# Kernel optimization log

Measured on AMD Instinct MI355X. Metric: run time of the kernel, lower is better.

Reference implementation:

```python
import jax, jax.numpy as jnp
import numpy as np

EMBED_DIM = 768
NUM_HEADS = 12


def setup_inputs() -> dict:
    key = jax.random.key(0)
    ks = jax.random.split(key, 9)
    C = EMBED_DIM
    x = jax.random.normal(ks[0], (8, 3136, C), dtype=jnp.float32)
    s = 0.02
    Wq = jax.random.normal(ks[1], (C, C), dtype=jnp.float32) * s
    Wk = jax.random.normal(ks[2], (C, C), dtype=jnp.float32) * s
    Wv = jax.random.normal(ks[3], (C, C), dtype=jnp.float32) * s
    Wo = jax.random.normal(ks[4], (C, C), dtype=jnp.float32) * s
    bq = jax.random.normal(ks[5], (C,), dtype=jnp.float32) * s
    bk = jax.random.normal(ks[6], (C,), dtype=jnp.float32) * s
    bv = jax.random.normal(ks[7], (C,), dtype=jnp.float32) * s
    bo = jax.random.normal(ks[8], (C,), dtype=jnp.float32) * s
    return {"x": x, "Wq": Wq, "bq": bq, "Wk": Wk, "bk": bk,
            "Wv": Wv, "bv": bv, "Wo": Wo, "bo": bo, "T": 16}


def reference(x, Wq, bq, Wk, bk, Wv, bv, Wo, bo, T):
    B, N, C = x.shape
    H = NUM_HEADS
    hd = C // H
    Hh = H // 2
    P = N // T
    scale = 1.0 / np.sqrt(hd).astype(np.float32)

    Q = (x @ Wq + bq).reshape(B, T, P, H, hd)
    K = (x @ Wk + bk).reshape(B, T, P, H, hd)
    V = (x @ Wv + bv).reshape(B, T, P, H, hd)

    # spatial attention: first Hh heads, attend over patches within each frame
    Qs, Ks, Vs = Q[..., :Hh, :], K[..., :Hh, :], V[..., :Hh, :]
    scores_s = jnp.einsum('btphd,btqhd->bthpq', Qs, Ks) * scale  # (B,T,Hh,P,P)
    ws = jax.nn.softmax(scores_s, axis=-1)
    out_s = jnp.einsum('bthpq,btqhd->btphd', ws, Vs)  # (B,T,P,Hh,hd)

    # temporal attention: last Hh heads, attend over frames at each patch
    Qt, Kt, Vt = Q[..., Hh:, :], K[..., Hh:, :], V[..., Hh:, :]
    scores_t = jnp.einsum('btphd,bsphd->bphts', Qt, Kt) * scale  # (B,P,Hh,T,T)
    wt = jax.nn.softmax(scores_t, axis=-1)
    out_t = jnp.einsum('bphts,bsphd->btphd', wt, Vt)  # (B,T,P,Hh,hd)

    out = jnp.concatenate([out_s, out_t], axis=3).reshape(B, N, C)
    return out @ Wo + bo
```

## Files before the change

kernel.cpp:

```cpp
#include <hip/hip_runtime.h>


typedef __attribute__((ext_vector_type(8))) short short8;
typedef __attribute__((ext_vector_type(4))) float f32x4;

typedef __attribute__((address_space(1))) void gvoid;
typedef __attribute__((address_space(3))) void lvoid;

__device__ __forceinline__ unsigned short f2b(float f) {
  unsigned int u = __float_as_uint(f);
  unsigned int r = (u + 0x7FFFu + ((u >> 16) & 1u)) >> 16;
  return (unsigned short)r;
}

__global__ __launch_bounds__(256) void k_convert_x(
    const float* __restrict__ x, unsigned short* __restrict__ xb,
    const float* __restrict__ bq, const float* __restrict__ bk,
    const float* __restrict__ bv, float* __restrict__ bqkv) {
  int tid = blockIdx.x * 256 + threadIdx.x;
  if (tid < 2304)
    bqkv[tid] = tid < 768 ? bq[tid] : (tid < 1536 ? bk[tid - 768] : bv[tid - 1536]);
  float4 v = ((const float4*)x)[tid];
  ushort4 o;
  o.x = f2b(v.x); o.y = f2b(v.y); o.z = f2b(v.z); o.w = f2b(v.w);
  ((ushort4*)xb)[tid] = o;
}

__global__ __launch_bounds__(256) void k_pack_w(
    const float* __restrict__ Wq, const float* __restrict__ Wk,
    const float* __restrict__ Wv, const float* __restrict__ Wo,
    unsigned short* __restrict__ wqkvT, unsigned short* __restrict__ woT) {
  __shared__ float tile[32][33];
  int bid = blockIdx.x;
  const float* W;
  unsigned short* dst;
  int n0, k0;
  if (bid < 1728) {
    int tn = bid % 72, tk = bid / 72;
    n0 = tn * 32; k0 = tk * 32;
    int which = n0 / 768;
    W = which == 0 ? Wq : (which == 1 ? Wk : Wv);
    dst = wqkvT;
  } else {
    int b2 = bid - 1728;
    int tn = b2 % 24, tk = b2 / 24;
    n0 = tn * 32; k0 = tk * 32;
    W = Wo; dst = woT;
  }
  int nn0 = n0 % 768;
  for (int i = threadIdx.x; i < 1024; i += 256) {
    int r = i >> 5, c = i & 31;
    tile[r][c] = W[(size_t)(k0 + r) * 768 + nn0 + c];
  }
  __syncthreads();
  for (int i = threadIdx.x; i < 1024; i += 256) {
    int r = i >> 5, c = i & 31;
    dst[(size_t)(n0 + r) * 768 + k0 + c] = f2b(tile[c][r]);
  }
}


#define FENCE asm volatile("" ::: "memory")
#define BARRIER do { FENCE; __builtin_amdgcn_s_barrier(); FENCE; } while (0)
#define WAIT_LGKM0 asm volatile("s_waitcnt lgkmcnt(0)" ::: "memory")
#define WAIT_VM6 asm volatile("s_waitcnt vmcnt(6)" ::: "memory")

#define STAGE(PBASE, BUFBASE, HT, KT_) do {                                          \
    int kt__ = (KT_);                                                                \
    bool real__ = (kt__ < 12);                                                       \
    if (!real__) kt__ -= 12;                                                         \
    const unsigned short* src__ = (PBASE) + (HT) * 98304 + kt__ * 64;                \
    unsigned d0__ = real__ ? ((BUFBASE) + (HT) * 8192 + w * 512) : (65536u + w * 512); \
    unsigned d1__ = real__ ? ((BUFBASE) + (HT) * 8192 + 4096 + w * 512) : (65536u + w * 512); \
    __builtin_amdgcn_global_load_lds((const gvoid*)src__, (lvoid*)(lds + d0__), 16, 0, 0); \
    __builtin_amdgcn_global_load_lds((const gvoid*)(src__ + 49152), (lvoid*)(lds + d1__), 16, 0, 0); \
  } while (0)

#define LDA(MH, ABASE) do {                                                          \
    const unsigned short* ab__ = lds + (ABASE) + ((MH) * 128 + arow) * 64;           \
    _Pragma("unroll")                                                                \
    for (int mf = 0; mf < 4; ++mf) {                                                 \
      af[mf][0] = *(const short8*)(ab__ + mf * 1024 + s0);                           \
      af[mf][1] = *(const short8*)(ab__ + mf * 1024 + s1);                           \
    }                                                                                \
  } while (0)

#define LDB(NH, BBASE) do {                                                          \
    const unsigned short* bb__ = lds + (BBASE) + ((NH) * 128 + brow) * 64;           \
    _Pragma("unroll")                                                                \
    for (int nf = 0; nf < 2; ++nf) {                                                 \
      bf[nf][0] = *(const short8*)(bb__ + nf * 1024 + s0);                           \
      bf[nf][1] = *(const short8*)(bb__ + nf * 1024 + s1);                           \
    }                                                                                \
  } while (0)

#define MM(MH, NH) do {                                                              \
    __builtin_amdgcn_s_setprio(1);                                                   \
    _Pragma("unroll")                                                                \
    for (int mf = 0; mf < 4; ++mf) {                                                 \
      _Pragma("unroll")                                                              \
      for (int nf = 0; nf < 2; ++nf) {                                               \
        acc[MH][mf][NH][nf] = __builtin_amdgcn_mfma_f32_16x16x32_bf16(               \
            af[mf][0], bf[nf][0], acc[MH][mf][NH][nf], 0, 0, 0);                     \
        acc[MH][mf][NH][nf] = __builtin_amdgcn_mfma_f32_16x16x32_bf16(               \
            af[mf][1], bf[nf][1], acc[MH][mf][NH][nf], 0, 0, 0);                     \
      }                                                                              \
    }                                                                                \
    __builtin_amdgcn_s_setprio(0);                                                   \
  } while (0)

__global__ __launch_bounds__(512, 2) void k_gemm256(
    const unsigned short* __restrict__ A, const unsigned short* __restrict__ Bt,
    const float* __restrict__ bias, unsigned short* __restrict__ Cout,
    int M, int N) {
  __shared__ __align__(16) unsigned short lds[69632];
  const int nwg = gridDim.x;
  const int nbx = N >> 8;
  const int orig = blockIdx.x;
  const int q = nwg >> 3, r = nwg & 7;
  const int xcd = orig & 7, lin = orig >> 3;
  const int wg = (xcd < r ? xcd * (q + 1) : r * (q + 1) + (xcd - r) * q) + lin;
  const int m0 = (wg / nbx) << 8, n0 = (wg % nbx) << 8;

  const int tid = threadIdx.x;
  const int w = tid >> 6, l = tid & 63;
  const int wm = w >> 2, wn = w & 3;
  const int lg = l >> 4, ln = l & 15;
  const int arow = wm * 64 + ln;
  const int brow = wn * 32 + ln;
  const int s0 = (lg ^ (ln & 7)) * 8;
  const int s1 = s0 ^ 32;
  const int srow = tid >> 3;
  const int slg8 = ((tid & 7) ^ (srow & 7)) * 8;
  const unsigned short* pA = A + (size_t)(m0 + srow) * 768 + slg8;
  const unsigned short* pB = Bt + (size_t)(n0 + srow) * 768 + slg8;

  f32x4 acc[2][4][2][2] = {};

  STAGE(pA, 0,     0, 0);
  STAGE(pB, 16384, 1, 0);
  STAGE(pA, 0,     1, 0);
  STAGE(pB, 16384, 0, 0);
  STAGE(pA, 32768, 0, 1);
  STAGE(pB, 49152, 1, 1);
  STAGE(pA, 32768, 1, 1);
  asm volatile("s_waitcnt vmcnt(6)" ::: "memory");
  __builtin_amdgcn_s_barrier();
  FENCE;

  for (int it = 0; it < 6; ++it) {
    const int kt1 = 2 * it + 1, ktn0 = 2 * it + 2, ktn1 = 2 * it + 3;
    short8 af[4][2], bf[2][2];
    LDA(0, 0); LDB(0, 16384);
    STAGE(pB, 49152, 0, kt1);
    BARRIER; WAIT_LGKM0; MM(0, 0); BARRIER;
    LDB(1, 16384);
    STAGE(pA, 0, 0, ktn0);
    BARRIER; WAIT_LGKM0; MM(0, 1); BARRIER;
    LDA(1, 0);
    STAGE(pB, 16384, 1, ktn0);
    BARRIER; WAIT_LGKM0; MM(1, 1); BARRIER;
    LDB(0, 16384);
    STAGE(pA, 0, 1, ktn0);
    WAIT_VM6;
    BARRIER; WAIT_LGKM0; MM(1, 0); BARRIER;
    LDA(0, 32768); LDB(0, 49152);
    STAGE(pB, 16384, 0, ktn0);
    BARRIER; WAIT_LGKM0; MM(0, 0); BARRIER;
    LDB(1, 49152);
    STAGE(pA, 32768, 0, ktn1);
    BARRIER; WAIT_LGKM0; MM(0, 1); BARRIER;
    LDA(1, 32768);
    STAGE(pB, 49152, 1, ktn1);
    BARRIER; WAIT_LGKM0; MM(1, 1); BARRIER;
    LDB(0, 49152);
    STAGE(pA, 32768, 1, ktn1);
    WAIT_VM6;
    BARRIER; WAIT_LGKM0; MM(1, 0); BARRIER;
  }

#pragma unroll
  for (int mh = 0; mh < 2; ++mh)
#pragma unroll
    for (int mf = 0; mf < 4; ++mf)
#pragma unroll
      for (int nh = 0; nh < 2; ++nh)
#pragma unroll
        for (int nf = 0; nf < 2; ++nf) {
          const int col = n0 + nh * 128 + wn * 32 + nf * 16 + ln;
          const float bval = bias[col];
          const int row = m0 + mh * 128 + wm * 64 + mf * 16 + lg * 4;
#pragma unroll
          for (int rr = 0; rr < 4; ++rr)
            Cout[(size_t)(row + rr) * N + col] = f2b(acc[mh][mf][nh][nf][rr] + bval);
        }
}

__global__ __launch_bounds__(256) void k_gemm_out(
    const unsigned short* __restrict__ A, const unsigned short* __restrict__ Bt,
    const float* __restrict__ bias, float* __restrict__ C,
    int M, int N, int K) {
  __shared__ __align__(16) unsigned short As[2][128 * 32];
  __shared__ __align__(16) unsigned short Bs[2][128 * 32];
  const int tid = threadIdx.x;
  const int w = tid >> 6, l = tid & 63;
  const int lg = l >> 4, ln = l & 15;
  const int m0 = blockIdx.y * 128, n0 = blockIdx.x * 128;
  const int wr = (w >> 1) * 64, wc = (w & 1) * 64;
  f32x4 acc[4][4] = {};
  const unsigned short* ga = A + (size_t)(m0 + (tid >> 2)) * K + ((tid & 3) * 8);
  const unsigned short* gb = Bt + (size_t)(n0 + (tid >> 2)) * K + ((tid & 3) * 8);
  const size_t krow64 = (size_t)64 * K;
  const int wofs = w * 512;

#define OSTAGE(CO, K0) do {                                                                        \
    __builtin_amdgcn_global_load_lds((const gvoid*)(ga + (K0)),          (lvoid*)(&As[0][0] + (CO) + wofs),        16, 0, 0); \
    __builtin_amdgcn_global_load_lds((const gvoid*)(ga + krow64 + (K0)), (lvoid*)(&As[0][0] + (CO) + 2048 + wofs), 16, 0, 0); \
    __builtin_amdgcn_global_load_lds((const gvoid*)(gb + (K0)),          (lvoid*)(&Bs[0][0] + (CO) + wofs),        16, 0, 0); \
    __builtin_amdgcn_global_load_lds((const gvoid*)(gb + krow64 + (K0)), (lvoid*)(&Bs[0][0] + (CO) + 2048 + wofs), 16, 0, 0); \
  } while (0)

  OSTAGE(0, 0);
  asm volatile("s_waitcnt vmcnt(0)" ::: "memory");
  BARRIER;
  int co = 0;
  for (int k0 = 0; k0 < K; k0 += 32) {
    if (k0 + 32 < K) OSTAGE(co ^ 4096, k0 + 32);
    const unsigned short* as = &As[0][0] + co;
    const unsigned short* bs = &Bs[0][0] + co;
    short8 a[4], b[4];
#pragma unroll
    for (int mt = 0; mt < 4; ++mt)
      a[mt] = *(const short8*)(as + (wr + mt * 16 + ln) * 32 + lg * 8);
#pragma unroll
    for (int nt = 0; nt < 4; ++nt)
      b[nt] = *(const short8*)(bs + (wc + nt * 16 + ln) * 32 + lg * 8);
#pragma unroll
    for (int mt = 0; mt < 4; ++mt)
#pragma unroll
      for (int nt = 0; nt < 4; ++nt)
        acc[mt][nt] = __builtin_amdgcn_mfma_f32_16x16x32_bf16(a[mt], b[nt], acc[mt][nt], 0, 0, 0);
    asm volatile("s_waitcnt vmcnt(0)" ::: "memory");
    BARRIER;
    co ^= 4096;
  }
#pragma unroll
  for (int nt = 0; nt < 4; ++nt) {
    int col = n0 + wc + nt * 16 + ln;
    float bval = bias[col];
#pragma unroll
    for (int mt = 0; mt < 4; ++mt) {
      int row = m0 + wr + mt * 16 + lg * 4;
#pragma unroll
      for (int r = 0; r < 4; ++r)
        C[(size_t)(row + r) * N + col] = acc[mt][nt][r] + bval;
    }
  }
#undef OSTAGE
}

__global__ __launch_bounds__(256) void k_attn_spatial(
    const unsigned short* __restrict__ qkv, unsigned short* __restrict__ attn) {
  const int bi = blockIdx.x;
  const int h = bi % 6;
  const int t = (bi / 6) % 16;
  const int b = bi / 96;
  const int base_row = b * 3136 + t * 196;
  __shared__ __align__(16) unsigned short Vt[64][232];
  __shared__ __align__(16) unsigned short Pl[4][16][232];
  for (int i = threadIdx.x; i < 196 * 64; i += 256) {
    int key = i >> 6, d = i & 63;
    Vt[d][key] = qkv[(size_t)(base_row + key) * 2304 + 1536 + h * 64 + d];
  }
  for (int i = threadIdx.x; i < 64 * 28; i += 256)
    Vt[i / 28][196 + (i % 28)] = 0;
  __syncthreads();
  const int w = threadIdx.x >> 6, l = threadIdx.x & 63;
  const int lg = l >> 4, ln = l & 15;
  const float scale = 0.125f;
  for (int mt = w; mt < 13; mt += 4) {
    int qm = mt * 16 + ln; if (qm > 195) qm = 195;
    const size_t qoff = (size_t)(base_row + qm) * 2304 + h * 64 + lg * 8;
    short8 qa0 = *(const short8*)(qkv + qoff);
    short8 qa1 = *(const short8*)(qkv + qoff + 32);
    f32x4 st[13];
#pragma unroll
    for (int nt = 0; nt < 13; ++nt) {
      int kn = nt * 16 + ln; if (kn > 195) kn = 195;
      const size_t koff = (size_t)(base_row + kn) * 2304 + 768 + h * 64 + lg * 8;
      short8 kb0 = *(const short8*)(qkv + koff);
      short8 kb1 = *(const short8*)(qkv + koff + 32);
      f32x4 s = {0.f, 0.f, 0.f, 0.f};
      s = __builtin_amdgcn_mfma_f32_16x16x32_bf16(qa0, kb0, s, 0, 0, 0);
      s = __builtin_amdgcn_mfma_f32_16x16x32_bf16(qa1, kb1, s, 0, 0, 0);
      st[nt] = s;
    }
    float mr[4] = {-1e30f, -1e30f, -1e30f, -1e30f};
#pragma unroll
    for (int nt = 0; nt < 13; ++nt) {
      bool valid = (nt * 16 + ln) < 196;
#pragma unroll
      for (int r = 0; r < 4; ++r) {
        float v = valid ? st[nt][r] * scale : -1e30f;
        st[nt][r] = v;
        mr[r] = fmaxf(mr[r], v);
      }
    }
#pragma unroll
    for (int msk = 1; msk <= 8; msk <<= 1)
#pragma unroll
      for (int r = 0; r < 4; ++r) mr[r] = fmaxf(mr[r], __shfl_xor(mr[r], msk));
    float sm[4] = {0.f, 0.f, 0.f, 0.f};
#pragma unroll
    for (int nt = 0; nt < 13; ++nt)
#pragma unroll
      for (int r = 0; r < 4; ++r) {
        float p = __expf(st[nt][r] - mr[r]);
        st[nt][r] = p;
        sm[r] += p;
      }
#pragma unroll
    for (int msk = 1; msk <= 8; msk <<= 1)
#pragma unroll
      for (int r = 0; r < 4; ++r) sm[r] += __shfl_xor(sm[r], msk);
    float inv[4];
#pragma unroll
    for (int r = 0; r < 4; ++r) inv[r] = 1.f / sm[r];
#pragma unroll
    for (int nt = 0; nt < 13; ++nt)
#pragma unroll
      for (int r = 0; r < 4; ++r)
        Pl[w][lg * 4 + r][nt * 16 + ln] = f2b(st[nt][r] * inv[r]);
#pragma unroll
    for (int r = 0; r < 4; ++r) Pl[w][ln][208 + lg * 4 + r] = 0;
#pragma unroll
    for (int nt4 = 0; nt4 < 4; ++nt4) {
      f32x4 acc = {0.f, 0.f, 0.f, 0.f};
#pragma unroll
      for (int ks = 0; ks < 7; ++ks) {
        short8 pa = *(const short8*)(&Pl[w][ln][ks * 32 + lg * 8]);
        short8 vb = *(const short8*)(&Vt[nt4 * 16 + ln][ks * 32 + lg * 8]);
        acc = __builtin_amdgcn_mfma_f32_16x16x32_bf16(pa, vb, acc, 0, 0, 0);
      }
#pragma unroll
      for (int r = 0; r < 4; ++r) {
        int m = mt * 16 + lg * 4 + r;
        if (m < 196)
          attn[(size_t)(base_row + m) * 768 + h * 64 + nt4 * 16 + ln] = f2b(acc[r]);
      }
    }
  }
}

__global__ __launch_bounds__(256) void k_attn_temporal(
    const unsigned short* __restrict__ qkv, unsigned short* __restrict__ attn) {
  const int w = threadIdx.x >> 6, l = threadIdx.x & 63;
  const int u = blockIdx.x * 4 + w;
  const int b = u / 1176;
  const int rem = u % 1176;
  const int p = rem / 6;
  const int h = 6 + rem % 6;
  const size_t rowb = (size_t)b * 3136 + p;
  __shared__ __align__(16) unsigned short Vt[4][64][40];
  __shared__ __align__(16) unsigned short Pl[4][16][40];
  for (int i = l; i < 1024; i += 64) {
    int tt = i >> 6, d = i & 63;
    Vt[w][d][tt] = qkv[(rowb + (size_t)tt * 196) * 2304 + 1536 + h * 64 + d];
  }
  for (int i = l; i < 1024; i += 64)
    Vt[w][i >> 4][16 + (i & 15)] = 0;
  const int lg = l >> 4, ln = l & 15;
  const size_t qoff = (rowb + (size_t)ln * 196) * 2304 + h * 64 + lg * 8;
  short8 qa0 = *(const short8*)(qkv + qoff);
  short8 qa1 = *(const short8*)(qkv + qoff + 32);
  short8 kb0 = *(const short8*)(qkv + qoff + 768);
  short8 kb1 = *(const short8*)(qkv + qoff + 768 + 32);
  f32x4 s = {0.f, 0.f, 0.f, 0.f};
  s = __builtin_amdgcn_mfma_f32_16x16x32_bf16(qa0, kb0, s, 0, 0, 0);
  s = __builtin_amdgcn_mfma_f32_16x16x32_bf16(qa1, kb1, s, 0, 0, 0);
  const float scale = 0.125f;
  float stv[4], mr[4];
#pragma unroll
  for (int r = 0; r < 4; ++r) { stv[r] = s[r] * scale; mr[r] = stv[r]; }
#pragma unroll
  for (int msk = 1; msk <= 8; msk <<= 1)
#pragma unroll
    for (int r = 0; r < 4; ++r) mr[r] = fmaxf(mr[r], __shfl_xor(mr[r], msk));
  float sm[4];
#pragma unroll
  for (int r = 0; r < 4; ++r) { stv[r] = __expf(stv[r] - mr[r]); sm[r] = stv[r]; }
#pragma unroll
  for (int msk = 1; msk <= 8; msk <<= 1)
#pragma unroll
    for (int r = 0; r < 4; ++r) sm[r] += __shfl_xor(sm[r], msk);
#pragma unroll
  for (int r = 0; r < 4; ++r)
    Pl[w][lg * 4 + r][ln] = f2b(stv[r] / sm[r]);
#pragma unroll
  for (int r = 0; r < 4; ++r) Pl[w][ln][16 + lg * 4 + r] = 0;
  short8 pa = *(const short8*)(&Pl[w][ln][lg * 8]);
#pragma unroll
  for (int nt4 = 0; nt4 < 4; ++nt4) {
    short8 vb = *(const short8*)(&Vt[w][nt4 * 16 + ln][lg * 8]);
    f32x4 acc = {0.f, 0.f, 0.f, 0.f};
    acc = __builtin_amdgcn_mfma_f32_16x16x32_bf16(pa, vb, acc, 0, 0, 0);
#pragma unroll
    for (int r = 0; r < 4; ++r) {
      int tq = lg * 4 + r;
      attn[((size_t)b * 3136 + (size_t)tq * 196 + p) * 768 + h * 64 + nt4 * 16 + ln] = f2b(acc[r]);
    }
  }
}

extern "C" void kernel_launch(void* const* d_in, const int* in_sizes, int n_in,
                              void* d_out, int out_size, void* d_ws, size_t ws_size,
                              hipStream_t stream) {
  const float* x  = (const float*)d_in[0];
  const float* Wq = (const float*)d_in[1];
  const float* bq = (const float*)d_in[2];
  const float* Wk = (const float*)d_in[3];
  const float* bk = (const float*)d_in[4];
  const float* Wv = (const float*)d_in[5];
  const float* bv = (const float*)d_in[6];
  const float* Wo = (const float*)d_in[7];
  const float* bo = (const float*)d_in[8];
  float* out = (float*)d_out;
  char* ws = (char*)d_ws;
  unsigned short* xb    = (unsigned short*)(ws + 0);
  unsigned short* wqkvT = (unsigned short*)(ws + 38535168);
  float*          bqkv  = (float*)(ws + 42074112);
  unsigned short* woT   = (unsigned short*)(ws + 42083328);
  unsigned short* qkvb  = (unsigned short*)(ws + 43262976);
  unsigned short* attnb = (unsigned short*)(ws + 158868480);

  k_convert_x<<<18816, 256, 0, stream>>>(x, xb, bq, bk, bv, bqkv);
  k_pack_w<<<2304, 256, 0, stream>>>(Wq, Wk, Wv, Wo, wqkvT, woT);
  k_gemm256<<<882, 512, 0, stream>>>(xb, wqkvT, bqkv, qkvb, 25088, 2304);
  k_attn_spatial<<<768, 256, 0, stream>>>(qkvb, attnb);
  k_attn_temporal<<<2352, 256, 0, stream>>>(qkvb, attnb);
  k_gemm_out<<<dim3(6, 196), 256, 0, stream>>>(attnb, woT, bo, out, 25088, 768, 768);
}
```

Before: 255.2 us.

## Halve barriers and double-buffer B fragments in bf16 GEMM main loop

Restructures the GEMM k-loop schedule. B fragments are kept in two register sets so the B(0) fragments can be reused across two MFMA phases without reloading, and the explicit lgkmcnt(0) waits plus the second barrier per phase are removed. Global-to-LDS staging is reordered with a vmcnt(4) wait in place of vmcnt(6). The intent is to cut synchronisation stalls and redundant LDS reads between MFMA clusters. The cost is more live registers, and dropping the lgkm waits and barriers risks LDS read/write races if the compiler's implicit waits do not cover them.

```diff
diff --git a/kernel.cpp b/kernel.cpp
--- a/kernel.cpp
+++ b/kernel.cpp
@@ -62,8 +62,7 @@
 
 #define FENCE asm volatile("" ::: "memory")
 #define BARRIER do { FENCE; __builtin_amdgcn_s_barrier(); FENCE; } while (0)
-#define WAIT_LGKM0 asm volatile("s_waitcnt lgkmcnt(0)" ::: "memory")
-#define WAIT_VM6 asm volatile("s_waitcnt vmcnt(6)" ::: "memory")
+#define WAIT_VM4 asm volatile("s_waitcnt vmcnt(4)" ::: "memory")
 
 #define STAGE(PBASE, BUFBASE, HT, KT_) do {                                          \
     int kt__ = (KT_);                                                                \
@@ -85,25 +84,25 @@
     }                                                                                \
   } while (0)
 
-#define LDB(NH, BBASE) do {                                                          \
+#define LDB(NH, BBASE, BF) do {                                                      \
     const unsigned short* bb__ = lds + (BBASE) + ((NH) * 128 + brow) * 64;           \
     _Pragma("unroll")                                                                \
     for (int nf = 0; nf < 2; ++nf) {                                                 \
-      bf[nf][0] = *(const short8*)(bb__ + nf * 1024 + s0);                           \
-      bf[nf][1] = *(const short8*)(bb__ + nf * 1024 + s1);                           \
+      BF[nf][0] = *(const short8*)(bb__ + nf * 1024 + s0);                           \
+      BF[nf][1] = *(const short8*)(bb__ + nf * 1024 + s1);                           \
     }                                                                                \
   } while (0)
 
-#define MM(MH, NH) do {                                                              \
+#define MM(MH, NH, BF) do {                                                          \
     __builtin_amdgcn_s_setprio(1);                                                   \
     _Pragma("unroll")                                                                \
     for (int mf = 0; mf < 4; ++mf) {                                                 \
       _Pragma("unroll")                                                              \
       for (int nf = 0; nf < 2; ++nf) {                                               \
         acc[MH][mf][NH][nf] = __builtin_amdgcn_mfma_f32_16x16x32_bf16(               \
-            af[mf][0], bf[nf][0], acc[MH][mf][NH][nf], 0, 0, 0);                     \
+            af[mf][0], BF[nf][0], acc[MH][mf][NH][nf], 0, 0, 0);                     \
         acc[MH][mf][NH][nf] = __builtin_amdgcn_mfma_f32_16x16x32_bf16(               \
-            af[mf][1], bf[nf][1], acc[MH][mf][NH][nf], 0, 0, 0);                     \
+            af[mf][1], BF[nf][1], acc[MH][mf][NH][nf], 0, 0, 0);                     \
       }                                                                              \
     }                                                                                \
     __builtin_amdgcn_s_setprio(0);                                                   \
@@ -138,45 +137,41 @@
   f32x4 acc[2][4][2][2] = {};
 
   STAGE(pA, 0,     0, 0);
+  STAGE(pB, 16384, 0, 0);
+  STAGE(pA, 0,     1, 0);
   STAGE(pB, 16384, 1, 0);
-  STAGE(pA, 0,     1, 0);
-  STAGE(pB, 16384, 0, 0);
   STAGE(pA, 32768, 0, 1);
   STAGE(pB, 49152, 1, 1);
-  STAGE(pA, 32768, 1, 1);
-  asm volatile("s_waitcnt vmcnt(6)" ::: "memory");
-  __builtin_amdgcn_s_barrier();
-  FENCE;
+  WAIT_VM4;
+  BARRIER;
 
   for (int it = 0; it < 6; ++it) {
     const int kt1 = 2 * it + 1, ktn0 = 2 * it + 2, ktn1 = 2 * it + 3;
-    short8 af[4][2], bf[2][2];
-    LDA(0, 0); LDB(0, 16384);
+    short8 af[4][2], bf0[2][2], bf1[2][2];
+    LDA(0, 0); LDB(0, 16384, bf0);
+    STAGE(pA, 32768, 1, kt1);
+    BARRIER; MM(0, 0, bf0);
+    LDB(1, 16384, bf1);
     STAGE(pB, 49152, 0, kt1);
-    BARRIER; WAIT_LGKM0; MM(0, 0); BARRIER;
-    LDB(1, 16384);
+    BARRIER; MM(0, 1, bf1);
+    LDA(1, 0);
     STAGE(pA, 0, 0, ktn0);
-    BARRIER; WAIT_LGKM0; MM(0, 1); BARRIER;
-    LDA(1, 0);
+    BARRIER; MM(1, 1, bf1);
     STAGE(pB, 16384, 1, ktn0);
-    BARRIER; WAIT_LGKM0; MM(1, 1); BARRIER;
-    LDB(0, 16384);
+    WAIT_VM4;
+    BARRIER; MM(1, 0, bf0);
+    LDA(0, 32768); LDB(0, 49152, bf0);
     STAGE(pA, 0, 1, ktn0);
-    WAIT_VM6;
-    BARRIER; WAIT_LGKM0; MM(1, 0); BARRIER;
-    LDA(0, 32768); LDB(0, 49152);
+    BARRIER; MM(0, 0, bf0);
+    LDB(1, 49152, bf1);
     STAGE(pB, 16384, 0, ktn0);
-    BARRIER; WAIT_LGKM0; MM(0, 0); BARRIER;
-    LDB(1, 49152);
+    BARRIER; MM(0, 1, bf1);
+    LDA(1, 32768);
     STAGE(pA, 32768, 0, ktn1);
-    BARRIER; WAIT_LGKM0; MM(0, 1); BARRIER;
-    LDA(1, 32768);
+    BARRIER; MM(1, 1, bf1);
     STAGE(pB, 49152, 1, ktn1);
-    BARRIER; WAIT_LGKM0; MM(1, 1); BARRIER;
-    LDB(0, 49152);
-    STAGE(pA, 32768, 1, ktn1);
-    WAIT_VM6;
-    BARRIER; WAIT_LGKM0; MM(1, 0); BARRIER;
+    WAIT_VM4;
+    BARRIER; MM(1, 0, bf0);
   }
 
 #pragma unroll
```

Result: slower. 261.8 us (+2.6%).
